# Kernel optimization log

Hardware: AMD Instinct MI355X
Metric: run time of the kernel (lower is better)

The kernel has to match this reference:

```python
import jax, jax.numpy as jnp
import numpy as np
import math

LOG2 = math.log(2)
B, N, H, E, M = 128, 2048, 300, 20, 200
IN = 3 * H + 3 * E  # 960: [mem, query, mem*query, 3 feature embs]
NEG = -10000.0


def _bucket(x):
    # floor(log2(x)) + 3 for x > 4, identity for x <= 4, clamped to [0, 9]
    xf = x.astype(jnp.float32)
    logspace = jnp.floor(jnp.log(jnp.maximum(xf, 1.0)) / LOG2).astype(jnp.int32) + 3
    return jnp.clip(jnp.where(x <= 4, x, logspace), 0, 9)


def setup_inputs() -> dict:
    key = jax.random.key(0)
    ks = jax.random.split(key, 12)
    return {
        "query_vector": jax.random.normal(ks[0], (B, H), jnp.float32),
        "ment_score": jax.random.normal(ks[1], (B,), jnp.float32),
        "mem_vectors": jax.random.normal(ks[2], (B, N, H), jnp.float32),
        "ent_counter": jax.random.randint(ks[3], (B, N), 0, 20, jnp.int32),
        "distances": jax.random.randint(ks[4], (B, N), 0, 5000, jnp.int32),
        "last_action_idx": jax.random.randint(ks[5], (B,), 0, 5, jnp.int32),
        "cell_idx": jax.random.randint(ks[6], (B,), 0, N, jnp.int32),
        "W1": jax.random.normal(ks[7], (IN, M), jnp.float32) / np.sqrt(IN),
        "b1": jnp.zeros((M,), jnp.float32),
        "W2": jax.random.normal(ks[8], (M, 1), jnp.float32) / np.sqrt(M),
        "b2": jnp.zeros((1,), jnp.float32),
        "dist_table": jax.random.normal(ks[9], (10, E), jnp.float32),
        "count_table": jax.random.normal(ks[10], (10, E), jnp.float32),
        "action_table": jax.random.normal(ks[11], (5, E), jnp.float32),
    }


def reference(query_vector, ment_score, mem_vectors, ent_counter, distances,
              last_action_idx, cell_idx, W1, b1, W2, b2,
              dist_table, count_table, action_table):
    # ---- feature embeddings (get_feature_embs, litbank: dist+counter+last_action) ----
    dist_emb = dist_table[_bucket(distances)]            # [B, N, E]
    cnt_emb = count_table[_bucket(ent_counter)]          # [B, N, E]
    act_emb = jnp.broadcast_to(action_table[last_action_idx][:, None, :], (B, N, E))
    feature_embs = jnp.concatenate([dist_emb, cnt_emb, act_emb], axis=-1)  # [B, N, 3E]

    # ---- get_coref_new_scores ----
    q = jnp.broadcast_to(query_vector[:, None, :], (B, N, H))
    pair_vec = jnp.concatenate([mem_vectors, q, mem_vectors * q, feature_embs], axis=-1)  # [B, N, IN]
    hdn = jax.nn.relu(jnp.einsum('bni,im->bnm', pair_vec, W1) + b1)
    pair_score = (jnp.einsum('bnm,mo->bno', hdn, W2) + b2)[..., 0]  # [B, N]
    coref_score = pair_score + ment_score[:, None]

    mask = (ent_counter > 0).astype(jnp.float32)                            # [B, N]
    full_mask = jnp.concatenate([mask, jnp.ones((B, 1), jnp.float32)], axis=1)
    full_score = jnp.concatenate([coref_score, jnp.zeros((B, 1), jnp.float32)], axis=1)
    coref_new_scores = full_score * full_mask + (1.0 - full_mask) * NEG     # [B, N+1]

    # ---- coref_update (entity_rep='max' default branch: running average + masked scatter) ----
    brange = jnp.arange(B)
    cnt_sel = ent_counter[brange, cell_idx].astype(jnp.float32)             # [B]
    mem_sel = mem_vectors[brange, cell_idx]                                 # [B, H]
    avg_vec = (mem_sel * cnt_sel[:, None] + query_vector) / (cnt_sel[:, None] + 1.0)
    onehot = (jnp.arange(N)[None, :] == cell_idx[:, None]).astype(jnp.float32)[:, :, None]  # [B, N, 1]
    new_mem = mem_vectors * (1.0 - onehot) + onehot * avg_vec[:, None, :]

    return coref_new_scores, new_mem
```

## Files before the change

kernel.cpp:

```cpp
#include <hip/hip_runtime.h>
#include <math.h>

#define BB 128
#define NN 2048
#define HH 300
#define EE 20
#define MM 200
#define NEGV (-10000.0f)
#define SCORES_OFF (BB * (NN + 1))

#define NCOL 208
#define KSTEPS 10
#define ROWSH 72
#define KIMG (NCOL * ROWSH)
#define CH16 (KIMG / 8)
#define BIMG_SHORTS ((size_t)BB * KSTEPS * KIMG)

typedef short bf16x8 __attribute__((ext_vector_type(8)));
typedef float f32x4 __attribute__((ext_vector_type(4)));

__device__ __forceinline__ int bucketf(int x) {
  if (x <= 4) return x < 0 ? 0 : x;
  float l = floorf(logf((float)x) / 0.69314718055994530942f);
  int bi = (int)l + 3;
  return bi > 9 ? 9 : bi;
}

__device__ __forceinline__ short f2bf(float f) {
  union { float f; unsigned u; } v; v.f = f;
  unsigned r = (v.u + 0x7FFFu + ((v.u >> 16) & 1u)) >> 16;
  return (short)r;
}
__device__ __forceinline__ float bf2f(short s) {
  union { unsigned u; float f; } v; v.u = ((unsigned)(unsigned short)s) << 16;
  return v.f;
}

__device__ __forceinline__ void gload16(const void* g, void* l) {
  __builtin_amdgcn_global_load_lds(
      (const __attribute__((address_space(1))) void*)g,
      (__attribute__((address_space(3))) void*)l, 16, 0, 0);
}

__global__ void k_prep2(const float* __restrict__ W1, const float* __restrict__ b1,
                        const float* __restrict__ q, const float* __restrict__ mem,
                        const float* __restrict__ dtab, const float* __restrict__ ctab,
                        const float* __restrict__ atab, const int* __restrict__ lact,
                        const int* __restrict__ entc, const int* __restrict__ cell,
                        float* __restrict__ distW, float* __restrict__ cntW,
                        float* __restrict__ bias, float* __restrict__ avg,
                        short* __restrict__ Bimg, float* __restrict__ out) {
  const int blk = blockIdx.x;
  const int tid = threadIdx.x;
  if (blk < 13) {
    int idx = blk * 320 + tid;
    if (idx >= 2 * 10 * MM) return;
    int t = idx / (10 * MM);
    int r = idx % (10 * MM);
    int d = r / MM;
    int m = r % MM;
    const float* tab = (t == 0) ? dtab : ctab;
    int wrow0 = (t == 0) ? (3 * HH) : (3 * HH + EE);
    float s = 0.f;
#pragma unroll
    for (int e = 0; e < EE; e++) s += tab[d * EE + e] * W1[(wrow0 + e) * MM + m];
    ((t == 0) ? distW : cntW)[d * MM + m] = s;
  } else if (blk < 93) {
    int idx = (blk - 13) * 320 + tid;
    if (idx >= BB * MM) return;
    int b = idx / MM;
    int m = idx % MM;
    float s = b1[m];
    for (int h = 0; h < HH; h++) s += q[b * HH + h] * W1[(HH + h) * MM + m];
    int la = lact[b];
#pragma unroll
    for (int e = 0; e < EE; e++)
      s += atab[la * EE + e] * W1[(3 * HH + 2 * EE + e) * MM + m];
    bias[idx] = s;
  } else if (blk < 221) {
    int b = blk - 93;
    int ci = cell[b];
    if (tid < HH) {
      float c = (float)entc[b * NN + ci];
      float m = mem[((size_t)b * NN + ci) * HH + tid];
      avg[b * HH + tid] = (m * c + q[b * HH + tid]) / (c + 1.f);
    } else if (tid == HH) {
      out[b * (NN + 1) + NN] = 0.f;
    }
  } else {
    int idx = (blk - 221) * 320 + tid;
    int col = idx % NCOL;
    int bks = idx / NCOL;
    int ks = bks % KSTEPS;
    int b = bks / KSTEPS;
    int k0 = ks * 32;
    const float* qb = q + b * HH;
    short* dst = Bimg + (size_t)idx * ROWSH;
#pragma unroll
    for (int g = 0; g < 4; g++) {
      bf16x8 h8, l8;
#pragma unroll
      for (int i = 0; i < 8; i++) {
        int k = k0 + 8 * g + i;
        float val = 0.f;
        if (k < HH && col < MM) {
          val = fmaf(qb[k], W1[(size_t)(2 * HH + k) * MM + col],
                     W1[(size_t)k * MM + col]);
        }
        short h = f2bf(val);
        h8[i] = h;
        l8[i] = f2bf(val - bf2f(h));
      }
      *(bf16x8*)(dst + g * 8) = h8;
      *(bf16x8*)(dst + 32 + g * 8) = l8;
    }
    *(bf16x8*)(dst + 64) = (bf16x8){0, 0, 0, 0, 0, 0, 0, 0};
  }
}

__device__ __forceinline__ void issueA(const float* rowp, int kb, float* va) {
  if (kb + 7 < HH) {
    float4 x0 = *(const float4*)(rowp + kb);
    float4 x1 = *(const float4*)(rowp + kb + 4);
    va[0] = x0.x; va[1] = x0.y; va[2] = x0.z; va[3] = x0.w;
    va[4] = x1.x; va[5] = x1.y; va[6] = x1.z; va[7] = x1.w;
  } else {
#pragma unroll
    for (int i = 0; i < 8; i++) {
      int k = kb + i;
      va[i] = (k < HH) ? rowp[k] : 0.f;
    }
  }
}

__device__ __forceinline__ void storeA(const float* va, int kb, float* orow,
                                       const float* avgp, bool subst) {
  if (kb + 7 < HH) {
    float4 o0, o1;
    if (subst) {
      o0 = *(const float4*)(avgp + kb);
      o1 = *(const float4*)(avgp + kb + 4);
    } else {
      o0 = make_float4(va[0], va[1], va[2], va[3]);
      o1 = make_float4(va[4], va[5], va[6], va[7]);
    }
    *(float4*)(orow + kb) = o0;
    *(float4*)(orow + kb + 4) = o1;
  } else {
#pragma unroll
    for (int i = 0; i < 8; i++) {
      int k = kb + i;
      if (k < HH) orow[k] = subst ? avgp[k] : va[i];
    }
  }
}

__device__ __forceinline__ void cvtA(const float* va, bf16x8* ahi, bf16x8* alo) {
#pragma unroll
  for (int i = 0; i < 8; i++) {
    short h = f2bf(va[i]);
    (*ahi)[i] = h;
    (*alo)[i] = f2bf(va[i] - bf2f(h));
  }
}

__device__ __forceinline__ void epilogue(
    const f32x4* acc, int b, int n0, int w, int lr, int g,
    const float* __restrict__ bias, const float* __restrict__ distW,
    const float* __restrict__ cntW, const float* __restrict__ W2,
    const float* __restrict__ b2, const float* __restrict__ ment,
    const int* __restrict__ entc, const int* __restrict__ dist,
    float* __restrict__ out) {
  const float addc = b2[0] + ment[b];
  const float* bi = bias + b * MM;
  float s[4];
#pragma unroll
  for (int r = 0; r < 4; r++) {
    int nr = n0 + w * 16 + 4 * g + r;
    int db = bucketf(dist[b * NN + nr]);
    int cb = bucketf(entc[b * NN + nr]);
    const float* dW = distW + db * MM;
    const float* cW = cntW + cb * MM;
    float acc_s = 0.f;
#pragma unroll
    for (int f = 0; f < 13; f++) {
      if (f < 12 || lr < 8) {
        int m = f * 16 + lr;
        float h = acc[f][r] + bi[m] + dW[m] + cW[m];
        acc_s += fmaxf(h, 0.f) * W2[m];
      }
    }
    s[r] = acc_s;
  }
#pragma unroll
  for (int off = 1; off < 16; off <<= 1) {
#pragma unroll
    for (int r = 0; r < 4; r++) s[r] += __shfl_xor(s[r], off);
  }
  if (lr == 0) {
#pragma unroll
    for (int r = 0; r < 4; r++) {
      int nr = n0 + w * 16 + 4 * g + r;
      int mk = entc[b * NN + nr] > 0;
      out[b * (NN + 1) + nr] = mk ? (s[r] + addc) : NEGV;
    }
  }
}

__global__ __launch_bounds__(512, 4) void k_main(
    const float* __restrict__ mem, const short* __restrict__ Bimg,
    const float* __restrict__ bias, const float* __restrict__ distW,
    const float* __restrict__ cntW, const float* __restrict__ W2,
    const float* __restrict__ b2, const float* __restrict__ ment,
    const int* __restrict__ entc, const int* __restrict__ dist,
    const int* __restrict__ cell, const float* __restrict__ avg,
    float* __restrict__ out) {
  __shared__ __align__(16) short btS[2][KIMG];

  const int tid = threadIdx.x;
  const int bid = blockIdx.x;
  const int b = (bid & 7) * 16 + (bid >> 7);
  const int n0 = ((bid >> 3) & 15) * 128;

  const int w = tid >> 6;
  const int l = tid & 63;
  const int lr = l & 15;
  const int g = l >> 4;

  const int ci = cell[b];
  const int n = n0 + w * 16 + lr;
  const float* rowp = mem + ((size_t)b * NN + n) * HH;
  float* orow = out + SCORES_OFF + ((size_t)b * NN + n) * HH;
  const float* avgp = avg + b * HH;
  const bool subst = (n == ci);
  const short* bsrc = Bimg + (size_t)b * KSTEPS * KIMG;

  f32x4 acc[13];
#pragma unroll
  for (int f = 0; f < 13; f++) acc[f] = (f32x4){0.f, 0.f, 0.f, 0.f};

  float va[8];
  issueA(rowp, 8 * g, va);
#pragma unroll
  for (int it = 0; it < 4; it++) {
    int i = tid + it * 512;
    if (i < CH16) gload16(bsrc + (size_t)i * 8, &btS[0][i * 8]);
  }
  bf16x8 ahi, alo;
  cvtA(va, &ahi, &alo);
  __syncthreads();

  for (int ks = 0; ks < KSTEPS; ks++) {
    const int cur = ks & 1;
    const int kb_cur = ks * 32 + 8 * g;
    float vn[8];
    if (ks < KSTEPS - 1) {
      const short* bs = bsrc + (size_t)(ks + 1) * KIMG;
#pragma unroll
      for (int it = 0; it < 4; it++) {
        int i = tid + it * 512;
        if (i < CH16) gload16(bs + (size_t)i * 8, &btS[cur ^ 1][i * 8]);
      }
      issueA(rowp, kb_cur + 32, vn);
    }
    storeA(va, kb_cur, orow, avgp, subst);

#pragma unroll
    for (int f = 0; f < 13; f++) {
      const short* bp = &btS[cur][(f * 16 + lr) * ROWSH + g * 8];
      bf16x8 bhi = *(const bf16x8*)bp;
      bf16x8 blo = *(const bf16x8*)(bp + 32);
      acc[f] = __builtin_amdgcn_mfma_f32_16x16x32_bf16(ahi, bhi, acc[f], 0, 0, 0);
      acc[f] = __builtin_amdgcn_mfma_f32_16x16x32_bf16(alo, bhi, acc[f], 0, 0, 0);
      acc[f] = __builtin_amdgcn_mfma_f32_16x16x32_bf16(ahi, blo, acc[f], 0, 0, 0);
    }

    if (ks < KSTEPS - 1) {
#pragma unroll
      for (int i = 0; i < 8; i++) va[i] = vn[i];
      cvtA(va, &ahi, &alo);
      __syncthreads();
    }
  }

  epilogue(acc, b, n0, w, lr, g, bias, distW, cntW, W2, b2, ment, entc, dist, out);
}

extern "C" void kernel_launch(void* const* d_in, const int* in_sizes, int n_in,
                              void* d_out, int out_size, void* d_ws, size_t ws_size,
                              hipStream_t stream) {
  const float* q    = (const float*)d_in[0];
  const float* ment = (const float*)d_in[1];
  const float* mem  = (const float*)d_in[2];
  const int* entc   = (const int*)d_in[3];
  const int* dist   = (const int*)d_in[4];
  const int* lact   = (const int*)d_in[5];
  const int* cell   = (const int*)d_in[6];
  const float* W1   = (const float*)d_in[7];
  const float* b1   = (const float*)d_in[8];
  const float* W2   = (const float*)d_in[9];
  const float* b2   = (const float*)d_in[10];
  const float* dtab = (const float*)d_in[11];
  const float* ctab = (const float*)d_in[12];
  const float* atab = (const float*)d_in[13];
  float* out = (float*)d_out;

  short* Bimg  = (short*)d_ws;
  float* fws   = (float*)(Bimg + BIMG_SHORTS);
  float* bias  = fws;
  float* distW = bias + BB * MM;
  float* cntW  = distW + 10 * MM;
  float* avg   = cntW + 10 * MM;

  k_prep2<<<1053, 320, 0, stream>>>(W1, b1, q, mem, dtab, ctab, atab, lact,
                                    entc, cell, distW, cntW, bias, avg, Bimg, out);
  k_main<<<2048, 512, 0, stream>>>(mem, Bimg, bias, distW, cntW, W2, b2, ment,
                                   entc, dist, cell, avg, out);
}
```

Before: 708.3 us.

## Deepen A-row prefetch to two steps ahead with explicit vmcnt waits

Fully unrolls the K loop and keeps three register buffers for the A rows, so global loads of mem rows are issued two k-steps ahead instead of one. It replaces __syncthreads with hand-placed s_waitcnt vmcnt counts, sched_barriers and raw s_barrier, aiming to keep more memory traffic in flight while the MFMAs run. In exchange it uses more registers, which may reduce occupancy under the launch bounds. The hard-coded vmcnt values must match the exact number of outstanding loads, or the code will read data before it has arrived.

After: 715.5 us. Within noise of the previous version (+1.0%).

```diff
diff --git a/kernel.cpp b/kernel.cpp
--- a/kernel.cpp
+++ b/kernel.cpp
@@ -207,6 +207,26 @@
   }
 }
 
+#define B_GLOADS(bufptr, bs)                                        \
+  {                                                                 \
+    _Pragma("unroll") for (int it = 0; it < 4; it++) {              \
+      int i = tid + it * 512;                                       \
+      if (i < CH16) gload16((bs) + (size_t)i * 8, (bufptr) + i * 8);\
+    }                                                               \
+  }
+
+#define MFMA_PHASE(bufptr)                                                         \
+  {                                                                                \
+    _Pragma("unroll") for (int f = 0; f < 13; f++) {                               \
+      const short* bp = (bufptr) + (f * 16 + lr) * ROWSH + g * 8;                  \
+      bf16x8 bhi = *(const bf16x8*)bp;                                             \
+      bf16x8 blo = *(const bf16x8*)(bp + 32);                                      \
+      acc[f] = __builtin_amdgcn_mfma_f32_16x16x32_bf16(ahi, bhi, acc[f], 0, 0, 0); \
+      acc[f] = __builtin_amdgcn_mfma_f32_16x16x32_bf16(alo, bhi, acc[f], 0, 0, 0); \
+      acc[f] = __builtin_amdgcn_mfma_f32_16x16x32_bf16(ahi, blo, acc[f], 0, 0, 0); \
+    }                                                                              \
+  }
+
 __global__ __launch_bounds__(512, 4) void k_main(
     const float* __restrict__ mem, const short* __restrict__ Bimg,
     const float* __restrict__ bias, const float* __restrict__ distW,
@@ -239,49 +259,45 @@
 #pragma unroll
   for (int f = 0; f < 13; f++) acc[f] = (f32x4){0.f, 0.f, 0.f, 0.f};
 
-  float va[8];
-  issueA(rowp, 8 * g, va);
-#pragma unroll
-  for (int it = 0; it < 4; it++) {
-    int i = tid + it * 512;
-    if (i < CH16) gload16(bsrc + (size_t)i * 8, &btS[0][i * 8]);
-  }
+  float va[3][8];
   bf16x8 ahi, alo;
-  cvtA(va, &ahi, &alo);
-  __syncthreads();
-
-  for (int ks = 0; ks < KSTEPS; ks++) {
-    const int cur = ks & 1;
-    const int kb_cur = ks * 32 + 8 * g;
-    float vn[8];
-    if (ks < KSTEPS - 1) {
-      const short* bs = bsrc + (size_t)(ks + 1) * KIMG;
-#pragma unroll
-      for (int it = 0; it < 4; it++) {
-        int i = tid + it * 512;
-        if (i < CH16) gload16(bs + (size_t)i * 8, &btS[cur ^ 1][i * 8]);
-      }
-      issueA(rowp, kb_cur + 32, vn);
-    }
-    storeA(va, kb_cur, orow, avgp, subst);
-
-#pragma unroll
-    for (int f = 0; f < 13; f++) {
-      const short* bp = &btS[cur][(f * 16 + lr) * ROWSH + g * 8];
-      bf16x8 bhi = *(const bf16x8*)bp;
-      bf16x8 blo = *(const bf16x8*)(bp + 32);
-      acc[f] = __builtin_amdgcn_mfma_f32_16x16x32_bf16(ahi, bhi, acc[f], 0, 0, 0);
-      acc[f] = __builtin_amdgcn_mfma_f32_16x16x32_bf16(alo, bhi, acc[f], 0, 0, 0);
-      acc[f] = __builtin_amdgcn_mfma_f32_16x16x32_bf16(ahi, blo, acc[f], 0, 0, 0);
-    }
-
-    if (ks < KSTEPS - 1) {
-#pragma unroll
-      for (int i = 0; i < 8; i++) va[i] = vn[i];
-      cvtA(va, &ahi, &alo);
-      __syncthreads();
-    }
-  }
+
+  issueA(rowp, 0 * 32 + 8 * g, va[0]);
+  B_GLOADS(&btS[0][0], bsrc);
+  issueA(rowp, 1 * 32 + 8 * g, va[1]);
+  asm volatile("s_waitcnt vmcnt(2)" ::: "memory");
+  __builtin_amdgcn_sched_barrier(0);
+  cvtA(va[0], &ahi, &alo);
+  __builtin_amdgcn_sched_barrier(0);
+  __builtin_amdgcn_s_barrier();
+  __builtin_amdgcn_sched_barrier(0);
+
+#pragma unroll
+  for (int ks = 0; ks < 8; ks++) {
+    B_GLOADS(&btS[(ks + 1) & 1][0], bsrc + (size_t)(ks + 1) * KIMG);
+    issueA(rowp, (ks + 2) * 32 + 8 * g, va[(ks + 2) % 3]);
+    storeA(va[ks % 3], ks * 32 + 8 * g, orow, avgp, subst);
+    MFMA_PHASE(&btS[ks & 1][0]);
+    asm volatile("s_waitcnt vmcnt(4)" ::: "memory");
+    __builtin_amdgcn_sched_barrier(0);
+    cvtA(va[(ks + 1) % 3], &ahi, &alo);
+    __builtin_amdgcn_sched_barrier(0);
+    __builtin_amdgcn_s_barrier();
+    __builtin_amdgcn_sched_barrier(0);
+  }
+
+  B_GLOADS(&btS[1][0], bsrc + (size_t)9 * KIMG);
+  storeA(va[8 % 3], 8 * 32 + 8 * g, orow, avgp, subst);
+  MFMA_PHASE(&btS[0][0]);
+  asm volatile("s_waitcnt vmcnt(2)" ::: "memory");
+  __builtin_amdgcn_sched_barrier(0);
+  cvtA(va[9 % 3], &ahi, &alo);
+  __builtin_amdgcn_sched_barrier(0);
+  __builtin_amdgcn_s_barrier();
+  __builtin_amdgcn_sched_barrier(0);
+
+  storeA(va[9 % 3], 9 * 32 + 8 * g, orow, avgp, subst);
+  MFMA_PHASE(&btS[1][0]);
 
   epilogue(acc, b, n0, w, lr, g, bias, distW, cntW, W2, b2, ment, entc, dist, out);
 }
```
